# Optimization experiments

Hardware: AMD Instinct MI355X
Metric: run time of the kernel (lower is better)

Reference implementation:

```python
import jax, jax.numpy as jnp
import numpy as np

N_NODES = 50000   # n_all_entities
N_EDGES = 800000  # nnz of sparse A_in (avg degree 16)
D = 96            # in_dim == out_dim
NEG_SLOPE = 0.01  # nn.LeakyReLU default


def setup_inputs() -> dict:
    key = jax.random.key(0)
    ks = jax.random.split(key, 8)
    ego = jax.random.normal(ks[0], (N_NODES, D), dtype=jnp.float32)
    a_rows = jax.random.randint(ks[1], (N_EDGES,), 0, N_NODES)
    a_cols = jax.random.randint(ks[2], (N_EDGES,), 0, N_NODES)
    a_vals = jax.random.uniform(ks[3], (N_EDGES,), dtype=jnp.float32)
    # torch Linear weights: shape (out_dim, in_dim), xavier-like scale
    scale = np.sqrt(2.0 / (D + D)).astype(np.float32)
    W1 = jax.random.normal(ks[4], (D, D), dtype=jnp.float32) * scale
    b1 = jnp.zeros((D,), dtype=jnp.float32)
    W2 = jax.random.normal(ks[5], (D, D), dtype=jnp.float32) * scale
    b2 = jnp.zeros((D,), dtype=jnp.float32)
    return {"ego": ego, "a_vals": a_vals, "W1": W1, "b1": b1,
            "W2": W2, "b2": b2, "a_rows": a_rows, "a_cols": a_cols}


def _leaky_relu(x):
    return jnp.where(x >= 0, x, NEG_SLOPE * x)


def reference(ego, a_vals, W1, b1, W2, b2, a_rows, a_cols):
    # side = A_in @ ego  (sparse COO matmul via gather + segment_sum)
    msgs = a_vals[:, None] * ego[a_cols]                      # [E, D]
    side = jax.ops.segment_sum(msgs, a_rows, num_segments=N_NODES)  # [N, D]
    # bi-interaction aggregator (dropout is identity in eval mode)
    sum_emb = _leaky_relu((ego + side) @ W1.T + b1)           # [N, D]
    bi_emb = _leaky_relu((ego * side) @ W2.T + b2)            # [N, D]
    return sum_emb + bi_emb
```

## Files before the change

### kernel.cpp

```cpp
#include <hip/hip_runtime.h>

#define NN 50000
#define NE 800000
#define DD 96
#define NEG 0.01f
#define FN 64
#define XST 104
#define NBK 196
#define BCAP 4600
#define EPA 4096
#define NBA 196
#define OVCAP 65536
#define QROW 128

typedef __attribute__((ext_vector_type(8))) short short8v;
typedef __attribute__((ext_vector_type(4))) float f32x4;

static __device__ __forceinline__ float lrelu(float x) {
  return (x >= 0.f) ? x : NEG * x;
}
static __device__ __forceinline__ unsigned short f2bf(float x) {
  unsigned u = __float_as_uint(x);
  u += 0x7fffu + ((u >> 16) & 1u);
  return (unsigned short)(u >> 16);
}
static __device__ __forceinline__ float bf2f(unsigned short h) {
  return __uint_as_float(((unsigned)h) << 16);
}
static __device__ __forceinline__ float bflo(unsigned u) {
  return __uint_as_float(u << 16);
}
static __device__ __forceinline__ float bfhi(unsigned u) {
  return __uint_as_float(u & 0xFFFF0000u);
}

__global__ __launch_bounds__(256) void scatter_kernel(
    const float* __restrict__ ego, const float* __restrict__ avals,
    const int* __restrict__ arows, const int* __restrict__ acols,
    float* __restrict__ side)
{
  int t = blockIdx.x * 256 + threadIdx.x;
  int e = t >> 5;
  int lane = t & 31;
  if (e >= NE) return;
  int row = arows[e];
  int col = acols[e];
  float v = avals[e];
  if (lane < 24) {
    const float4* src = (const float4*)(ego + (size_t)col * DD);
    float4 x = src[lane];
    float* dst = side + (size_t)row * DD + lane * 4;
    unsafeAtomicAdd(dst + 0, v * x.x);
    unsafeAtomicAdd(dst + 1, v * x.y);
    unsafeAtomicAdd(dst + 2, v * x.z);
    unsafeAtomicAdd(dst + 3, v * x.w);
  }
}

__global__ __launch_bounds__(192) void fuse_fb_kernel(
    const float* __restrict__ ego, const float* __restrict__ side,
    const float* __restrict__ W1, const float* __restrict__ b1,
    const float* __restrict__ W2, const float* __restrict__ b2,
    float* __restrict__ out)
{
  __shared__ float W1t[DD * DD];
  __shared__ float W2t[DD * DD];
  __shared__ float b1s[DD], b2s[DD];
  __shared__ float xs[192], ys[192];
  int tid = threadIdx.x;
  for (int i = tid; i < DD * DD; i += 192) {
    int j = i / DD, k = i - j * DD;
    W1t[k * DD + j] = W1[i];
    W2t[k * DD + j] = W2[i];
  }
  if (tid < DD) { b1s[tid] = b1[tid]; b2s[tid] = b2[tid]; }
  __syncthreads();
  int nl = tid / DD, j = tid - nl * DD;
  for (int p = blockIdx.x; p < NN / 2; p += gridDim.x) {
    int base = p * 192;
    float e = ego[base + tid], s = side[base + tid];
    xs[tid] = e + s; ys[tid] = e * s;
    __syncthreads();
    float a1 = b1s[j], a2 = b2s[j];
    const float* xr = xs + nl * DD;
    const float* yr = ys + nl * DD;
#pragma unroll 16
    for (int k = 0; k < DD; ++k) {
      a1 += xr[k] * W1t[k * DD + j];
      a2 += yr[k] * W2t[k * DD + j];
    }
    float r = lrelu(a1) + lrelu(a2);
    __syncthreads();
    out[base + tid] = r;
  }
}

#define NB_W   ((DD * DD) / 256)
#define NB_Q   ((NN + 63) / 64)
__global__ __launch_bounds__(256) void build_kernel(
    const int* __restrict__ rows, const int* __restrict__ cols,
    const float* __restrict__ vals,
    int* __restrict__ bptr, int* __restrict__ ovcur,
    int2* __restrict__ ovbuf, int2* __restrict__ buckets,
    const float* __restrict__ W1, const float* __restrict__ W2,
    unsigned short* __restrict__ Wb1, unsigned short* __restrict__ Wb2,
    const float* __restrict__ ego, unsigned char* __restrict__ egoq)
{
  __shared__ unsigned sw0[EPA];
  __shared__ unsigned sw1[EPA];
  __shared__ unsigned char sbid[EPA];
  __shared__ int bcnt[256], bofs[256], gbase[256], stmp[256];

  int blk = blockIdx.x;
  int tid = threadIdx.x;

  if (blk >= NBA) {
    int b = blk - NBA;
    if (b < NB_W) {
      int i = b * 256 + tid;
      Wb1[i] = f2bf(W1[i]);
      Wb2[i] = f2bf(W2[i]);
    } else {
      int r_loc = tid >> 2, q = tid & 3;
      int row = (b - NB_W) * 64 + r_loc;
      if (row < NN) {
        float4 f[6];
        const float4* src = (const float4*)(ego + (size_t)row * DD + q * 24);
#pragma unroll
        for (int t = 0; t < 6; ++t) f[t] = src[t];
        float m = 0.f;
#pragma unroll
        for (int t = 0; t < 6; ++t) {
          m = fmaxf(m, fmaxf(fmaxf(fabsf(f[t].x), fabsf(f[t].y)),
                             fmaxf(fabsf(f[t].z), fabsf(f[t].w))));
        }
        m = fmaxf(m, __shfl_xor(m, 1, 64));
        m = fmaxf(m, __shfl_xor(m, 2, 64));
        m = fmaxf(m, 1e-20f);
        float inv = 127.0f / m;
        unsigned* dst = (unsigned*)(egoq + (size_t)row * QROW + 4) + q * 6;
#pragma unroll
        for (int t = 0; t < 6; ++t) {
          int q0 = __float2int_rn(f[t].x * inv);
          int q1 = __float2int_rn(f[t].y * inv);
          int q2 = __float2int_rn(f[t].z * inv);
          int q3 = __float2int_rn(f[t].w * inv);
          dst[t] = (unsigned)(q0 & 255) | ((unsigned)(q1 & 255) << 8) |
                   ((unsigned)(q2 & 255) << 16) | ((unsigned)(q3 & 255) << 24);
        }
        if (q == 0) *(float*)(egoq + (size_t)row * QROW) = m * (1.0f / 127.0f);
      }
    }
    return;
  }

  int base = blk * EPA;
  int cnt_here = min(EPA, NE - base);

  bcnt[tid] = 0;
  __syncthreads();

  unsigned w0[16], w1[16];
  int bb[16], lp[16];
#pragma unroll
  for (int k = 0; k < 16; ++k) {
    int i = tid + k * 256;
    bb[k] = -1;
    if (i < cnt_here) {
      int e = base + i;
      int r = rows[e], c = cols[e];
      float v = vals[e];
      int b = r >> 8;
      bb[k] = b;
      w0[k] = (unsigned)c | ((unsigned)(r & 255) << 16) | ((unsigned)b << 24);
      w1[k] = (unsigned)f2bf(v);
      lp[k] = atomicAdd(&bcnt[b], 1);
    }
  }
  __syncthreads();

  int v = bcnt[tid];
  stmp[tid] = v;
  __syncthreads();
  for (int off = 1; off < 256; off <<= 1) {
    int add = (tid >= off) ? stmp[tid - off] : 0;
    __syncthreads();
    stmp[tid] += add;
    __syncthreads();
  }
  bofs[tid] = stmp[tid] - v;
  gbase[tid] = (tid < NBK && v > 0) ? atomicAdd(&bptr[tid], v) : 0;
  __syncthreads();

#pragma unroll
  for (int k = 0; k < 16; ++k) {
    if (bb[k] >= 0) {
      int s = bofs[bb[k]] + lp[k];
      sw0[s] = w0[k];
      sw1[s] = w1[k];
      sbid[s] = (unsigned char)bb[k];
    }
  }
  __syncthreads();

  for (int i = tid; i < cnt_here; i += 256) {
    int b = sbid[i];
    int off = i - bofs[b];
    int g = gbase[b] + off;
    int2 ent = make_int2((int)sw0[i], (int)sw1[i]);
    if (g < BCAP) {
      buckets[(size_t)b * BCAP + g] = ent;
    } else {
      int op = atomicAdd(ovcur, 1);
      if (op < OVCAP) ovbuf[op] = ent;
    }
  }
}

__global__ __launch_bounds__(256) void binB_kernel(
    const int2* __restrict__ buckets, const int* __restrict__ bptr,
    const int* __restrict__ ovcur, const int2* __restrict__ ovbuf,
    unsigned* __restrict__ cv, int* __restrict__ row_start)
{
  __shared__ int rcnt[256], rofs[256], rcur[256], stmp[256], sexc[256];
  int b = blockIdx.x, tid = threadIdx.x;

  int bv = (tid < NBK) ? bptr[tid] : 0;
  stmp[tid] = bv;
  __syncthreads();
  for (int off = 1; off < 256; off <<= 1) {
    int add = (tid >= off) ? stmp[tid - off] : 0;
    __syncthreads();
    stmp[tid] += add;
    __syncthreads();
  }
  sexc[tid] = stmp[tid] - bv;
  __syncthreads();
  int cvb = sexc[b];
  int total = bptr[b];
  int nreg = min(total, BCAP);
  int nov = min(*ovcur, OVCAP);
  const int2* reg = buckets + (size_t)b * BCAP;

  rcnt[tid] = 0;
  __syncthreads();

  for (int i = tid; i < nreg; i += 256) {
    unsigned w0 = (unsigned)reg[i].x;
    atomicAdd(&rcnt[(w0 >> 16) & 255], 1);
  }
  for (int i = tid; i < nov; i += 256) {
    unsigned w0 = (unsigned)ovbuf[i].x;
    if ((w0 >> 24) == (unsigned)b) atomicAdd(&rcnt[(w0 >> 16) & 255], 1);
  }
  __syncthreads();

  int v = rcnt[tid];
  stmp[tid] = v;
  __syncthreads();
  for (int off = 1; off < 256; off <<= 1) {
    int add = (tid >= off) ? stmp[tid - off] : 0;
    __syncthreads();
    stmp[tid] += add;
    __syncthreads();
  }
  rofs[tid] = stmp[tid] - v;
  rcur[tid] = rofs[tid];
  int grow = b * 256 + tid;
  if (grow <= NN) row_start[grow] = cvb + rofs[tid];
  __syncthreads();

  for (int i = tid; i < nreg; i += 256) {
    unsigned w0 = (unsigned)reg[i].x;
    unsigned w1 = (unsigned)reg[i].y;
    int rl = (w0 >> 16) & 255;
    int p = atomicAdd(&rcur[rl], 1);
    cv[cvb + p] = (w0 & 0xFFFFu) | (w1 << 16);
  }
  for (int i = tid; i < nov; i += 256) {
    unsigned w0 = (unsigned)ovbuf[i].x;
    unsigned w1 = (unsigned)ovbuf[i].y;
    if ((w0 >> 24) == (unsigned)b) {
      int rl = (w0 >> 16) & 255;
      int p = atomicAdd(&rcur[rl], 1);
      cv[cvb + p] = (w0 & 0xFFFFu) | (w1 << 16);
    }
  }
}

__global__ __launch_bounds__(256) void agg_kernel(
    const unsigned char* __restrict__ egoq, const int* __restrict__ row_start,
    const unsigned* __restrict__ cv, unsigned* __restrict__ sideb) {
  int wid = threadIdx.x >> 6, lane = threadIdx.x & 63;
  int row = blockIdx.x * 4 + wid;
  if (row >= NN) return;
  int s = row_start[row], e = row_start[row + 1];
  int half = lane >> 5, hl = lane & 31;
  float4 a[8];
#pragma unroll
  for (int d = 0; d < 8; ++d) a[d] = make_float4(0.f, 0.f, 0.f, 0.f);

  for (int base = s; base < e; base += 64) {
    int idx = base + lane;
    unsigned pk = 0;
    if (idx < e) pk = cv[idx];
    int n = min(64, e - base);
    for (int i = 0; i < n; i += 16) {
#pragma unroll
      for (int d = 0; d < 8; ++d) {
        unsigned p = __shfl(pk, i + 2 * d + half, 64);
        float v = bfhi(p);
        const char* rowp = (const char*)egoq + ((size_t)(p & 0xFFFFu) << 7);
        if (hl < 24) {
          float sc = *(const float*)rowp;
          unsigned u = *(const unsigned*)(rowp + 4 + hl * 4);
          float vs = v * sc;
          a[d].x += vs * (float)((int)(signed char)(u & 0xFF));
          a[d].y += vs * (float)((int)(signed char)((u >> 8) & 0xFF));
          a[d].z += vs * (float)((int)(signed char)((u >> 16) & 0xFF));
          a[d].w += vs * (float)(((int)u) >> 24);
        }
      }
    }
  }
  float4 acc;
  acc.x = ((a[0].x + a[1].x) + (a[2].x + a[3].x)) + ((a[4].x + a[5].x) + (a[6].x + a[7].x));
  acc.y = ((a[0].y + a[1].y) + (a[2].y + a[3].y)) + ((a[4].y + a[5].y) + (a[6].y + a[7].y));
  acc.z = ((a[0].z + a[1].z) + (a[2].z + a[3].z)) + ((a[4].z + a[5].z) + (a[6].z + a[7].z));
  acc.w = ((a[0].w + a[1].w) + (a[2].w + a[3].w)) + ((a[4].w + a[5].w) + (a[6].w + a[7].w));
  acc.x += __shfl(acc.x, lane ^ 32, 64);
  acc.y += __shfl(acc.y, lane ^ 32, 64);
  acc.z += __shfl(acc.z, lane ^ 32, 64);
  acc.w += __shfl(acc.w, lane ^ 32, 64);
  if (half == 0 && hl < 24) {
    unsigned lo = (unsigned)f2bf(acc.x) | ((unsigned)f2bf(acc.y) << 16);
    unsigned hi = (unsigned)f2bf(acc.z) | ((unsigned)f2bf(acc.w) << 16);
    *(uint2*)(sideb + (size_t)row * 48 + hl * 2) = make_uint2(lo, hi);
  }
}

__global__ __launch_bounds__(256) void fuse4_kernel(
    const unsigned char* __restrict__ egoq, const unsigned* __restrict__ sideb,
    const unsigned short* __restrict__ Wb1, const unsigned short* __restrict__ Wb2,
    const float* __restrict__ b1, const float* __restrict__ b2,
    float* __restrict__ out)
{
  __shared__ unsigned short xs[FN * XST];
  __shared__ unsigned short ys[FN * XST];
  int tid = threadIdx.x;
  int nbase = blockIdx.x * FN;

  for (int i = tid; i < FN * 24; i += 256) {
    int r = i / 24, u = i - r * 24;
    float e0 = 0.f, e1 = 0.f, e2 = 0.f, e3 = 0.f;
    float s0 = 0.f, s1 = 0.f, s2 = 0.f, s3 = 0.f;
    if (nbase + r < NN) {
      const char* rowp = (const char*)egoq + ((size_t)(nbase + r) << 7);
      float sc = *(const float*)rowp;
      unsigned uq = *(const unsigned*)(rowp + 4 + u * 4);
      e0 = sc * (float)((int)(signed char)(uq & 0xFF));
      e1 = sc * (float)((int)(signed char)((uq >> 8) & 0xFF));
      e2 = sc * (float)((int)(signed char)((uq >> 16) & 0xFF));
      e3 = sc * (float)(((int)uq) >> 24);
      uint2 sv = *(const uint2*)(sideb + (size_t)(nbase + r) * 48 + u * 2);
      s0 = bflo(sv.x); s1 = bfhi(sv.x);
      s2 = bflo(sv.y); s3 = bfhi(sv.y);
    }
    unsigned xlo = (unsigned)f2bf(e0 + s0) | ((unsigned)f2bf(e1 + s1) << 16);
    unsigned xhi = (unsigned)f2bf(e2 + s2) | ((unsigned)f2bf(e3 + s3) << 16);
    unsigned ylo = (unsigned)f2bf(e0 * s0) | ((unsigned)f2bf(e1 * s1) << 16);
    unsigned yhi = (unsigned)f2bf(e2 * s2) | ((unsigned)f2bf(e3 * s3) << 16);
    *(uint2*)(xs + r * XST + u * 4) = make_uint2(xlo, xhi);
    *(uint2*)(ys + r * XST + u * 4) = make_uint2(ylo, yhi);
  }
  __syncthreads();

  int w = tid >> 6, l = tid & 63;
  int lrow = l & 15, lk = l >> 4;

  f32x4 acc1[6], acc2[6];
#pragma unroll
  for (int t = 0; t < 6; ++t) {
    acc1[t] = (f32x4){0.f, 0.f, 0.f, 0.f};
    acc2[t] = (f32x4){0.f, 0.f, 0.f, 0.f};
  }

  const unsigned short* xrow = xs + (w * 16 + lrow) * XST + lk * 8;
  const unsigned short* yrow = ys + (w * 16 + lrow) * XST + lk * 8;

#pragma unroll
  for (int kk = 0; kk < 3; ++kk) {
    short8v ax = *(const short8v*)(xrow + kk * 32);
    short8v ay = *(const short8v*)(yrow + kk * 32);
    int kb = kk * 32 + lk * 8;
#pragma unroll
    for (int t = 0; t < 6; ++t) {
      int j = t * 16 + lrow;
      short8v bw1 = *(const short8v*)(Wb1 + j * DD + kb);
      short8v bw2 = *(const short8v*)(Wb2 + j * DD + kb);
      acc1[t] = __builtin_amdgcn_mfma_f32_16x16x32_bf16(ax, bw1, acc1[t], 0, 0, 0);
      acc2[t] = __builtin_amdgcn_mfma_f32_16x16x32_bf16(ay, bw2, acc2[t], 0, 0, 0);
    }
  }

  int node0 = nbase + w * 16 + lk * 4;
#pragma unroll
  for (int t = 0; t < 6; ++t) {
    int j = t * 16 + lrow;
    float bb1 = b1[j], bb2 = b2[j];
#pragma unroll
    for (int i = 0; i < 4; ++i) {
      int node = node0 + i;
      if (node < NN)
        out[(size_t)node * DD + j] = lrelu(acc1[t][i] + bb1) + lrelu(acc2[t][i] + bb2);
    }
  }
}

extern "C" void kernel_launch(void* const* d_in, const int* in_sizes, int n_in,
                              void* d_out, int out_size, void* d_ws, size_t ws_size,
                              hipStream_t stream) {
  const float* ego   = (const float*)d_in[0];
  const float* avals = (const float*)d_in[1];
  const float* W1    = (const float*)d_in[2];
  const float* b1    = (const float*)d_in[3];
  const float* W2    = (const float*)d_in[4];
  const float* b2    = (const float*)d_in[5];
  const int* arows   = (const int*)d_in[6];
  const int* acols   = (const int*)d_in[7];
  float* out = (float*)d_out;

  size_t off = 0;
  auto bump = [&](size_t bytes) {
    size_t o = off;
    off += (bytes + 1023) & ~(size_t)1023;
    return o;
  };
  char* ws = (char*)d_ws;
  size_t o_rs    = bump((size_t)(NN + 1) * 4);
  size_t o_cv    = bump((size_t)NE * 4);
  size_t o_wb1   = bump((size_t)DD * DD * 2);
  size_t o_wb2   = bump((size_t)DD * DD * 2);
  size_t o_egoq  = bump((size_t)NN * QROW);
  size_t o_bptr  = bump((size_t)(NBK + 1) * 4);
  size_t o_ovbuf = bump((size_t)OVCAP * 8);
  size_t o_sideb = bump((size_t)NN * DD * 2);
  size_t need = off;
  static_assert((size_t)NBK * BCAP * 8 <= (size_t)NN * DD * 2, "buckets fit in sideb");

  if (ws_size >= need) {
    int*  rs    = (int*)(ws + o_rs);
    unsigned* cv = (unsigned*)(ws + o_cv);
    unsigned short* Wb1  = (unsigned short*)(ws + o_wb1);
    unsigned short* Wb2  = (unsigned short*)(ws + o_wb2);
    unsigned char* egoq  = (unsigned char*)(ws + o_egoq);
    int*  bptr  = (int*)(ws + o_bptr);
    int*  ovcur = bptr + NBK;
    int2* ovbuf = (int2*)(ws + o_ovbuf);
    unsigned* sideb = (unsigned*)(ws + o_sideb);
    int2* buckets = (int2*)(ws + o_sideb);

    hipMemsetAsync(bptr, 0, (size_t)(NBK + 1) * 4, stream);
    build_kernel<<<NBA + NB_W + NB_Q, 256, 0, stream>>>(
        arows, acols, avals, bptr, ovcur, ovbuf, buckets,
        W1, W2, Wb1, Wb2, ego, egoq);
    binB_kernel<<<NBK, 256, 0, stream>>>(buckets, bptr, ovcur, ovbuf, cv, rs);
    agg_kernel<<<(NN + 3) / 4, 256, 0, stream>>>(egoq, rs, cv, sideb);
    fuse4_kernel<<<(NN + FN - 1) / FN, 256, 0, stream>>>(
        egoq, sideb, Wb1, Wb2, b1, b2, out);
  } else {
    size_t side_bytes = (size_t)NN * DD * sizeof(float);
    float* side = (ws_size >= side_bytes) ? (float*)d_ws : out;
    hipMemsetAsync(side, 0, side_bytes, stream);
    long long nthreads = (long long)NE * 32;
    int blocks = (int)((nthreads + 255) / 256);
    scatter_kernel<<<blocks, 256, 0, stream>>>(ego, avals, arows, acols, side);
    fuse_fb_kernel<<<1024, 192, 0, stream>>>(ego, side, W1, b1, W2, b2, out);
  }
}
```

Before: 99.48 us.

## Widen int8 gathers in aggregation, move row scale to tail, stage buckets in LDS

The quantized ego row layout moves the per-row scale to the end of the 128-byte row, so the int8 payload is 8-byte aligned. The aggregation kernel now has each 16-lane quarter handle one edge, with 12 lanes each loading 8 bytes. Four edges are gathered per step with independent loads, and the partial sums are combined by xor-shuffle reductions. This aims to cut the number of load instructions and raise memory-level parallelism. The binning kernel also copies each bucket into shared memory once instead of reading global memory twice, at the cost of about 37KB of LDS per block.

```diff
diff --git a/kernel.cpp b/kernel.cpp
--- a/kernel.cpp
+++ b/kernel.cpp
@@ -32,6 +32,9 @@
 }
 static __device__ __forceinline__ float bfhi(unsigned u) {
   return __uint_as_float(u & 0xFFFF0000u);
+}
+static __device__ __forceinline__ float sb(unsigned u, int k) {
+  return (float)((int)(signed char)((u >> (8 * k)) & 0xFF));
 }
 
 __global__ __launch_bounds__(256) void scatter_kernel(
@@ -138,7 +141,7 @@
         m = fmaxf(m, __shfl_xor(m, 2, 64));
         m = fmaxf(m, 1e-20f);
         float inv = 127.0f / m;
-        unsigned* dst = (unsigned*)(egoq + (size_t)row * QROW + 4) + q * 6;
+        unsigned* dst = (unsigned*)(egoq + (size_t)row * QROW) + q * 6;
 #pragma unroll
         for (int t = 0; t < 6; ++t) {
           int q0 = __float2int_rn(f[t].x * inv);
@@ -148,7 +151,7 @@
           dst[t] = (unsigned)(q0 & 255) | ((unsigned)(q1 & 255) << 8) |
                    ((unsigned)(q2 & 255) << 16) | ((unsigned)(q3 & 255) << 24);
         }
-        if (q == 0) *(float*)(egoq + (size_t)row * QROW) = m * (1.0f / 127.0f);
+        if (q == 0) *(float*)(egoq + (size_t)row * QROW + DD) = m * (1.0f / 127.0f);
       }
     }
     return;
@@ -222,6 +225,7 @@
     const int* __restrict__ ovcur, const int2* __restrict__ ovbuf,
     unsigned* __restrict__ cv, int* __restrict__ row_start)
 {
+  __shared__ int2 sent[BCAP];
   __shared__ int rcnt[256], rofs[256], rcur[256], stmp[256], sexc[256];
   int b = blockIdx.x, tid = threadIdx.x;
 
@@ -243,10 +247,11 @@
   const int2* reg = buckets + (size_t)b * BCAP;
 
   rcnt[tid] = 0;
+  for (int i = tid; i < nreg; i += 256) sent[i] = reg[i];
   __syncthreads();
 
   for (int i = tid; i < nreg; i += 256) {
-    unsigned w0 = (unsigned)reg[i].x;
+    unsigned w0 = (unsigned)sent[i].x;
     atomicAdd(&rcnt[(w0 >> 16) & 255], 1);
   }
   for (int i = tid; i < nov; i += 256) {
@@ -271,8 +276,8 @@
   __syncthreads();
 
   for (int i = tid; i < nreg; i += 256) {
-    unsigned w0 = (unsigned)reg[i].x;
-    unsigned w1 = (unsigned)reg[i].y;
+    unsigned w0 = (unsigned)sent[i].x;
+    unsigned w1 = (unsigned)sent[i].y;
     int rl = (w0 >> 16) & 255;
     int p = atomicAdd(&rcur[rl], 1);
     cv[cvb + p] = (w0 & 0xFFFFu) | (w1 << 16);
@@ -295,10 +300,15 @@
   int row = blockIdx.x * 4 + wid;
   if (row >= NN) return;
   int s = row_start[row], e = row_start[row + 1];
-  int half = lane >> 5, hl = lane & 31;
-  float4 a[8];
-#pragma unroll
-  for (int d = 0; d < 8; ++d) a[d] = make_float4(0.f, 0.f, 0.f, 0.f);
+  int q = lane >> 4, ql = lane & 15;
+  bool act = ql < 12;
+  int ql8 = ql * 8;
+
+  float a[4][8];
+#pragma unroll
+  for (int d = 0; d < 4; ++d)
+#pragma unroll
+    for (int j = 0; j < 8; ++j) a[d][j] = 0.f;
 
   for (int base = s; base < e; base += 64) {
     int idx = base + lane;
@@ -306,36 +316,51 @@
     if (idx < e) pk = cv[idx];
     int n = min(64, e - base);
     for (int i = 0; i < n; i += 16) {
-#pragma unroll
-      for (int d = 0; d < 8; ++d) {
-        unsigned p = __shfl(pk, i + 2 * d + half, 64);
-        float v = bfhi(p);
-        const char* rowp = (const char*)egoq + ((size_t)(p & 0xFFFFu) << 7);
-        if (hl < 24) {
-          float sc = *(const float*)rowp;
-          unsigned u = *(const unsigned*)(rowp + 4 + hl * 4);
-          float vs = v * sc;
-          a[d].x += vs * (float)((int)(signed char)(u & 0xFF));
-          a[d].y += vs * (float)((int)(signed char)((u >> 8) & 0xFF));
-          a[d].z += vs * (float)((int)(signed char)((u >> 16) & 0xFF));
-          a[d].w += vs * (float)(((int)u) >> 24);
+      unsigned p[4];
+#pragma unroll
+      for (int d = 0; d < 4; ++d) p[d] = __shfl(pk, i + 4 * d + q, 64);
+      uint2 u[4];
+      float sc[4];
+#pragma unroll
+      for (int d = 0; d < 4; ++d) {
+        const char* rowp = (const char*)egoq + ((size_t)(p[d] & 0xFFFFu) << 7);
+        if (act) {
+          u[d] = *(const uint2*)(rowp + ql8);
+          sc[d] = *(const float*)(rowp + DD);
+        } else {
+          u[d] = make_uint2(0u, 0u);
+          sc[d] = 0.f;
         }
       }
-    }
-  }
-  float4 acc;
-  acc.x = ((a[0].x + a[1].x) + (a[2].x + a[3].x)) + ((a[4].x + a[5].x) + (a[6].x + a[7].x));
-  acc.y = ((a[0].y + a[1].y) + (a[2].y + a[3].y)) + ((a[4].y + a[5].y) + (a[6].y + a[7].y));
-  acc.z = ((a[0].z + a[1].z) + (a[2].z + a[3].z)) + ((a[4].z + a[5].z) + (a[6].z + a[7].z));
-  acc.w = ((a[0].w + a[1].w) + (a[2].w + a[3].w)) + ((a[4].w + a[5].w) + (a[6].w + a[7].w));
-  acc.x += __shfl(acc.x, lane ^ 32, 64);
-  acc.y += __shfl(acc.y, lane ^ 32, 64);
-  acc.z += __shfl(acc.z, lane ^ 32, 64);
-  acc.w += __shfl(acc.w, lane ^ 32, 64);
-  if (half == 0 && hl < 24) {
-    unsigned lo = (unsigned)f2bf(acc.x) | ((unsigned)f2bf(acc.y) << 16);
-    unsigned hi = (unsigned)f2bf(acc.z) | ((unsigned)f2bf(acc.w) << 16);
-    *(uint2*)(sideb + (size_t)row * 48 + hl * 2) = make_uint2(lo, hi);
+#pragma unroll
+      for (int d = 0; d < 4; ++d) {
+        float vs = bfhi(p[d]) * sc[d];
+        a[d][0] += vs * sb(u[d].x, 0);
+        a[d][1] += vs * sb(u[d].x, 1);
+        a[d][2] += vs * sb(u[d].x, 2);
+        a[d][3] += vs * sb(u[d].x, 3);
+        a[d][4] += vs * sb(u[d].y, 0);
+        a[d][5] += vs * sb(u[d].y, 1);
+        a[d][6] += vs * sb(u[d].y, 2);
+        a[d][7] += vs * sb(u[d].y, 3);
+      }
+    }
+  }
+
+  float r[8];
+#pragma unroll
+  for (int j = 0; j < 8; ++j) {
+    r[j] = (a[0][j] + a[1][j]) + (a[2][j] + a[3][j]);
+    r[j] += __shfl_xor(r[j], 16, 64);
+    r[j] += __shfl_xor(r[j], 32, 64);
+  }
+  if (q == 0 && act) {
+    uint4 o;
+    o.x = (unsigned)f2bf(r[0]) | ((unsigned)f2bf(r[1]) << 16);
+    o.y = (unsigned)f2bf(r[2]) | ((unsigned)f2bf(r[3]) << 16);
+    o.z = (unsigned)f2bf(r[4]) | ((unsigned)f2bf(r[5]) << 16);
+    o.w = (unsigned)f2bf(r[6]) | ((unsigned)f2bf(r[7]) << 16);
+    *(uint4*)(sideb + (size_t)row * 48 + ql * 4) = o;
   }
 }
 
@@ -356,12 +381,12 @@
     float s0 = 0.f, s1 = 0.f, s2 = 0.f, s3 = 0.f;
     if (nbase + r < NN) {
       const char* rowp = (const char*)egoq + ((size_t)(nbase + r) << 7);
-      float sc = *(const float*)rowp;
-      unsigned uq = *(const unsigned*)(rowp + 4 + u * 4);
-      e0 = sc * (float)((int)(signed char)(uq & 0xFF));
-      e1 = sc * (float)((int)(signed char)((uq >> 8) & 0xFF));
-      e2 = sc * (float)((int)(signed char)((uq >> 16) & 0xFF));
-      e3 = sc * (float)(((int)uq) >> 24);
+      float sc = *(const float*)(rowp + DD);
+      unsigned uq = *(const unsigned*)(rowp + u * 4);
+      e0 = sc * sb(uq, 0);
+      e1 = sc * sb(uq, 1);
+      e2 = sc * sb(uq, 2);
+      e3 = sc * sb(uq, 3);
       uint2 sv = *(const uint2*)(sideb + (size_t)(nbase + r) * 48 + u * 2);
       s0 = bflo(sv.x); s1 = bfhi(sv.x);
       s2 = bflo(sv.y); s3 = bfhi(sv.y);
```

Measured after the change: 83.91 us. 1.19x faster.
